# Kernel tuning notes

Hardware: AMD Instinct MI355X
Metric: run time of the kernel (lower is better)

Reference implementation:

```python
import jax, jax.numpy as jnp
import numpy as np

N_PARTICLES = 10_000_000
GRID_N = 256  # per-axis grid size
GRID_EDGE = 10.0  # grid spans [-10, 10] in each axis


def setup_inputs() -> dict:
    key = jax.random.key(0)
    k1, k2 = jax.random.split(key)
    # uniform in [-11, 11]: some particles fall outside the grid -> exercises bounds mask
    positions = jax.random.uniform(k1, (N_PARTICLES, 3), dtype=jnp.float32,
                                   minval=-11.0, maxval=11.0)
    weights = jax.random.uniform(k2, (N_PARTICLES,), dtype=jnp.float32)
    return {"positions": positions, "weights": weights}


def reference(positions, weights):
    # Grid buffers (from Grid.__init__ with grid_edges=(10,10,10), n=(256,256,256))
    n = GRID_N
    grid_min = jnp.full((3,), -GRID_EDGE, dtype=positions.dtype)
    grid_max = jnp.full((3,), GRID_EDGE, dtype=positions.dtype)
    dx = (grid_max - grid_min) / (n - 1)  # [3]

    # float index: fi = (pos - min)/dx  -> nearest grid point via trunc(fi + 0.5)
    fi = (positions - grid_min[None, :]) / dx[None, :]          # [N,3]
    i = (fi + 0.5).astype(jnp.int32)  # C-style trunc-toward-zero, matches torch .type(int64)

    gd = jnp.all((i >= 0) & (i < n), axis=1)                    # [N] in-grid mask

    # flatten 3D index; out-of-grid particles routed to index 0 with zero weight
    flat = (i[:, 0] * n + i[:, 1]) * n + i[:, 2]                # [N]
    flat = jnp.where(gd, flat, 0)
    w = jnp.where(gd, weights, jnp.zeros_like(weights))

    grid = jnp.zeros((n * n * n,), dtype=positions.dtype).at[flat].add(w)
    return grid.reshape(n, n, n)
```

## Files before the change

### kernel.cpp

```cpp
#include <hip/hip_runtime.h>
#include <stdint.h>


constexpr int GRID_N = 256;
constexpr int SB     = 1024;
constexpr int CELLS  = 16384;
constexpr int NB     = 256;
constexpr int BT13   = 1024;
constexpr int RING   = 16;
constexpr int RSTR   = 17;
constexpr int SIDE_CAP = 4096;

__device__ __forceinline__ int particle_flat(float px, float py, float pz) {
#pragma clang fp contract(off)
    float fix = (px + 10.0f) * 12.75f;
    float fiy = (py + 10.0f) * 12.75f;
    float fiz = (pz + 10.0f) * 12.75f;
    int ix = (int)(fix + 0.5f);
    int iy = (int)(fiy + 0.5f);
    int iz = (int)(fiz + 0.5f);
    bool in = (ix >= 0) & (ix < GRID_N) &
              (iy >= 0) & (iy < GRID_N) &
              (iz >= 0) & (iz < GRID_N);
    return in ? ((ix << 16) | (iy << 8) | iz) : -1;
}

__global__ __launch_bounds__(BT13) void k1_hist(const float* __restrict__ pos,
                                                uint32_t* __restrict__ hist,
                                                int n)
{
    __shared__ uint32_t h[SB];
    for (int i = threadIdx.x; i < SB; i += BT13) h[i] = 0;
    __syncthreads();

    const float4* p4 = (const float4*)pos;
    int ngroups = n >> 2;
    int G = gridDim.x * BT13;
    for (int g = blockIdx.x * BT13 + threadIdx.x; g < ngroups; g += G) {
        float4 a = p4[(size_t)g * 3 + 0];
        float4 b = p4[(size_t)g * 3 + 1];
        float4 c = p4[(size_t)g * 3 + 2];
        int f0 = particle_flat(a.x, a.y, a.z);
        int f1 = particle_flat(a.w, b.x, b.y);
        int f2 = particle_flat(b.z, b.w, c.x);
        int f3 = particle_flat(c.y, c.z, c.w);
        if (f0 >= 0) atomicAdd(&h[f0 >> 14], 1u);
        if (f1 >= 0) atomicAdd(&h[f1 >> 14], 1u);
        if (f2 >= 0) atomicAdd(&h[f2 >> 14], 1u);
        if (f3 >= 0) atomicAdd(&h[f3 >> 14], 1u);
    }
    if (blockIdx.x == 0 && threadIdx.x == 0) {
        for (int p = n & ~3; p < n; ++p) {
            int f = particle_flat(pos[3 * p], pos[3 * p + 1], pos[3 * p + 2]);
            if (f >= 0) atomicAdd(&h[f >> 14], 1u);
        }
    }
    __syncthreads();
    uint32_t* out = hist + (size_t)blockIdx.x * SB;
    for (int i = threadIdx.x; i < SB; i += BT13) out[i] = h[i];
}

__global__ __launch_bounds__(128) void k2a_colscan(const uint32_t* __restrict__ hist,
                                                   uint32_t* __restrict__ offs,
                                                   uint32_t* __restrict__ totals,
                                                   int round8)
{
    int b = blockIdx.x * 128 + threadIdx.x;
    uint32_t run = 0;
    for (int blk = 0; blk < NB; blk += 8) {
        uint32_t v[8];
#pragma unroll
        for (int j = 0; j < 8; ++j) {
            uint32_t c = hist[(size_t)(blk + j) * SB + b];
            v[j] = round8 ? ((c + 7u) & ~7u) : c;
        }
#pragma unroll
        for (int j = 0; j < 8; ++j) {
            offs[(size_t)(blk + j) * SB + b] = run;
            run += v[j];
        }
    }
    totals[b] = run;
}

__global__ __launch_bounds__(256) void k2b_scan(const uint32_t* __restrict__ totals,
                                                uint32_t* __restrict__ base)
{
    __shared__ uint32_t part[256];
    int t = threadIdx.x;
    uint32_t local[4];
    uint32_t s = 0;
#pragma unroll
    for (int j = 0; j < 4; ++j) { local[j] = totals[t * 4 + j]; s += local[j]; }
    part[t] = s;
    __syncthreads();
    if (t == 0) {
        uint32_t run = 0;
        for (int i = 0; i < 256; ++i) { uint32_t tmp = part[i]; part[i] = run; run += tmp; }
    }
    __syncthreads();
    uint32_t run = part[t];
#pragma unroll
    for (int j = 0; j < 4; ++j) { base[t * 4 + j] = run; run += local[j]; }
    if (t == 255) base[SB] = run;
}

__global__ __launch_bounds__(BT13, 1) void k3_stage(
    const float* __restrict__ pos, const float* __restrict__ wgt,
    const uint32_t* __restrict__ offs, const uint32_t* __restrict__ base,
    uint2* __restrict__ pairs, uint2* __restrict__ sideg, int n)
{
    __shared__ uint2    stg[SB][RSTR];
    __shared__ uint32_t s_total[SB];
    __shared__ uint32_t s_flushed[SB];
    __shared__ uint32_t s_pbase[SB];
    __shared__ uint32_t s_wl[SB];
    __shared__ uint32_t s_wln;
    __shared__ uint32_t s_siden;

    const int tid = threadIdx.x;
    const int blk = blockIdx.x;

    s_total[tid]   = 0;
    s_flushed[tid] = 0;
    s_pbase[tid]   = base[tid] + offs[(size_t)blk * SB + tid];
    if (tid == 0) { s_wln = 0; s_siden = 0; }
    __syncthreads();

    uint2* side = sideg + (size_t)blk * SIDE_CAP;

    const float4* p4 = (const float4*)pos;
    const float4* w4 = (const float4*)wgt;
    int ngroups = n >> 2;
    int G = NB * BT13;
    int iters = (ngroups + G - 1) / G;

    for (int it = 0; it < iters; ++it) {
        int g = blk * BT13 + tid + it * G;
        if (g < ngroups) {
            float4 a = p4[(size_t)g * 3 + 0];
            float4 b = p4[(size_t)g * 3 + 1];
            float4 c = p4[(size_t)g * 3 + 2];
            float4 w = w4[g];
            int   f[4]  = { particle_flat(a.x, a.y, a.z), particle_flat(a.w, b.x, b.y),
                            particle_flat(b.z, b.w, c.x), particle_flat(c.y, c.z, c.w) };
            float ww[4] = { w.x, w.y, w.z, w.w };
#pragma unroll
            for (int k = 0; k < 4; ++k) {
                int fk = f[k];
                if (fk >= 0) {
                    uint32_t bin  = (uint32_t)fk >> 14;
                    uint32_t slot = atomicAdd(&s_total[bin], 1u);
                    if (slot - s_flushed[bin] < (uint32_t)RING) {
                        stg[bin][slot & (RING - 1)] =
                            make_uint2((uint32_t)fk & (CELLS - 1), __float_as_uint(ww[k]));
                    } else {
                        atomicSub(&s_total[bin], 1u);
                        uint32_t si = atomicAdd(&s_siden, 1u);
                        if (si < SIDE_CAP)
                            side[si] = make_uint2((uint32_t)fk, __float_as_uint(ww[k]));
                    }
                }
            }
        }
        __syncthreads();
        {
            uint32_t p = s_total[tid] - s_flushed[tid];
            if (p >= 8u) {
                uint32_t o = s_flushed[tid];
                s_wl[atomicAdd(&s_wln, 1u)] = ((uint32_t)tid << 22) | o;
                s_flushed[tid] = o + 8u;
            }
        }
        __syncthreads();
        {
            uint32_t m = s_wln;
            for (uint32_t j = tid; j < m * 8u; j += BT13) {
                uint32_t e   = s_wl[j >> 3];
                uint32_t bin = e >> 22;
                uint32_t o   = e & 0x3FFFFFu;
                uint32_t idx = o + (j & 7u);
                uint2 v = stg[bin][idx & (RING - 1)];
                uint64_t v64 = (uint64_t)v.x | ((uint64_t)v.y << 32);
                __builtin_nontemporal_store(v64,
                    (uint64_t*)&pairs[(size_t)s_pbase[bin] + idx]);
            }
            if (tid == 0) s_wln = 0;
        }
        __syncthreads();
    }

    if (tid == 0) {
        uint32_t ns = s_siden < (uint32_t)SIDE_CAP ? s_siden : (uint32_t)SIDE_CAP;
        for (uint32_t i = 0; i < ns; ++i) {
            uint2 e = side[i];
            uint32_t bin = e.x >> 14;
            while (s_total[bin] - s_flushed[bin] >= (uint32_t)RING) {
                uint32_t o = s_flushed[bin];
                for (int j = 0; j < 8; ++j)
                    pairs[(size_t)s_pbase[bin] + o + j] = stg[bin][(o + j) & (RING - 1)];
                s_flushed[bin] = o + 8u;
            }
            uint32_t slot = s_total[bin]++;
            stg[bin][slot & (RING - 1)] = make_uint2(e.x & (CELLS - 1), e.y);
        }
        if (blk == 0) {
            for (int p = n & ~3; p < n; ++p) {
                int f = particle_flat(pos[3 * p], pos[3 * p + 1], pos[3 * p + 2]);
                if (f >= 0) {
                    uint32_t bin = (uint32_t)f >> 14;
                    while (s_total[bin] - s_flushed[bin] >= (uint32_t)RING) {
                        uint32_t o = s_flushed[bin];
                        for (int j = 0; j < 8; ++j)
                            pairs[(size_t)s_pbase[bin] + o + j] = stg[bin][(o + j) & (RING - 1)];
                        s_flushed[bin] = o + 8u;
                    }
                    uint32_t slot = s_total[bin]++;
                    stg[bin][slot & (RING - 1)] =
                        make_uint2((uint32_t)f & (CELLS - 1), __float_as_uint(wgt[p]));
                }
            }
        }
    }
    __syncthreads();

    {
        uint32_t t = s_total[tid];
        uint32_t p = t - s_flushed[tid];
        uint32_t pad = ((p + 7u) & ~7u) - p;
        for (uint32_t j = 0; j < pad; ++j)
            stg[tid][(t + j) & (RING - 1)] = make_uint2(0u, 0u);
        s_total[tid] = t + pad;
    }
    __syncthreads();

    for (int r = 0; r < 2; ++r) {
        {
            uint32_t p = s_total[tid] - s_flushed[tid];
            if (p >= 8u) {
                uint32_t o = s_flushed[tid];
                s_wl[atomicAdd(&s_wln, 1u)] = ((uint32_t)tid << 22) | o;
                s_flushed[tid] = o + 8u;
            }
        }
        __syncthreads();
        {
            uint32_t m = s_wln;
            for (uint32_t j = tid; j < m * 8u; j += BT13) {
                uint32_t e   = s_wl[j >> 3];
                uint32_t bin = e >> 22;
                uint32_t o   = e & 0x3FFFFFu;
                uint32_t idx = o + (j & 7u);
                uint2 v = stg[bin][idx & (RING - 1)];
                uint64_t v64 = (uint64_t)v.x | ((uint64_t)v.y << 32);
                __builtin_nontemporal_store(v64,
                    (uint64_t*)&pairs[(size_t)s_pbase[bin] + idx]);
            }
        }
        __syncthreads();
        if (tid == 0) s_wln = 0;
        __syncthreads();
    }
}

__global__ __launch_bounds__(BT13) void k3_scatter(const float* __restrict__ pos,
                                                   const float* __restrict__ wgt,
                                                   const uint32_t* __restrict__ offs,
                                                   const uint32_t* __restrict__ base,
                                                   uint2* __restrict__ pairs,
                                                   int n)
{
    __shared__ uint32_t cur[SB];
    for (int i = threadIdx.x; i < SB; i += BT13)
        cur[i] = base[i] + offs[(size_t)blockIdx.x * SB + i];
    __syncthreads();

    const float4* p4 = (const float4*)pos;
    const float4* w4 = (const float4*)wgt;
    int ngroups = n >> 2;
    int G = gridDim.x * BT13;
    for (int g = blockIdx.x * BT13 + threadIdx.x; g < ngroups; g += G) {
        float4 a = p4[(size_t)g * 3 + 0];
        float4 b = p4[(size_t)g * 3 + 1];
        float4 c = p4[(size_t)g * 3 + 2];
        float4 w = w4[g];
        int   f[4]  = { particle_flat(a.x, a.y, a.z), particle_flat(a.w, b.x, b.y),
                        particle_flat(b.z, b.w, c.x), particle_flat(c.y, c.z, c.w) };
        float ww[4] = { w.x, w.y, w.z, w.w };
#pragma unroll
        for (int k = 0; k < 4; ++k) {
            if (f[k] >= 0) {
                uint32_t slot = atomicAdd(&cur[f[k] >> 14], 1u);
                pairs[slot] = make_uint2((uint32_t)(f[k] & (CELLS - 1)),
                                         __float_as_uint(ww[k]));
            }
        }
    }
    if (blockIdx.x == 0 && threadIdx.x == 0) {
        for (int p = n & ~3; p < n; ++p) {
            int f = particle_flat(pos[3 * p], pos[3 * p + 1], pos[3 * p + 2]);
            if (f >= 0) {
                uint32_t slot = atomicAdd(&cur[f >> 14], 1u);
                pairs[slot] = make_uint2((uint32_t)(f & (CELLS - 1)),
                                         __float_as_uint(wgt[p]));
            }
        }
    }
}

__global__ __launch_bounds__(BT13) void k4_accum(const uint2* __restrict__ pairs,
                                                 const uint32_t* __restrict__ base,
                                                 float* __restrict__ grid)
{
    __shared__ float acc[CELLS];
    for (int i = threadIdx.x; i < CELLS; i += BT13) acc[i] = 0.0f;
    __syncthreads();

    int b = blockIdx.x;
    uint32_t s = base[b], e = base[b + 1];
    for (uint32_t i = s + threadIdx.x; i < e; i += BT13) {
        uint2 p = pairs[i];
        atomicAdd(&acc[p.x], __uint_as_float(p.y));
    }
    __syncthreads();

    float4* out4 = (float4*)(grid + (size_t)b * CELLS);
    const float4* a4 = (const float4*)acc;
    for (int i = threadIdx.x; i < CELLS / 4; i += BT13) out4[i] = a4[i];
}

__global__ __launch_bounds__(256) void forcegrid_scatter_atomic(
    const float* __restrict__ pos, const float* __restrict__ wgt,
    float* __restrict__ grid, int n)
{
    int t = blockIdx.x * blockDim.x + threadIdx.x;
    long long bse = (long long)t * 4;
    if (bse >= n) return;
    const float4* p4 = (const float4*)pos;
    float4 a = p4[(size_t)t * 3 + 0];
    float4 b = p4[(size_t)t * 3 + 1];
    float4 c = p4[(size_t)t * 3 + 2];
    float4 w = ((const float4*)wgt)[t];
    int   f[4]  = { particle_flat(a.x, a.y, a.z), particle_flat(a.w, b.x, b.y),
                    particle_flat(b.z, b.w, c.x), particle_flat(c.y, c.z, c.w) };
    float ww[4] = { w.x, w.y, w.z, w.w };
#pragma unroll
    for (int k = 0; k < 4; ++k) {
        if (bse + k >= n) break;
        if (f[k] >= 0) atomicAdd(&grid[f[k]], ww[k]);
    }
}

extern "C" void kernel_launch(void* const* d_in, const int* in_sizes, int n_in,
                              void* d_out, int out_size, void* d_ws, size_t ws_size,
                              hipStream_t stream)
{
    const float* pos = (const float*)d_in[0];
    const float* wgt = (const float*)d_in[1];
    float* grid = (float*)d_out;
    int n = in_sizes[0] / 3;

    size_t npad = (size_t)n + (size_t)NB * SB * 7;
    size_t o1 = 0;
    uint2*    pairs1  = (uint2*)d_ws;                         o1 += npad * sizeof(uint2);
    uint2*    sideg   = (uint2*)((char*)d_ws + o1);           o1 += (size_t)NB * SIDE_CAP * sizeof(uint2);
    uint32_t* hist1   = (uint32_t*)((char*)d_ws + o1);        o1 += (size_t)NB * SB * 4;
    uint32_t* offs1   = (uint32_t*)((char*)d_ws + o1);        o1 += (size_t)NB * SB * 4;
    uint32_t* totals1 = (uint32_t*)((char*)d_ws + o1);        o1 += (size_t)SB * 4;
    uint32_t* base1   = (uint32_t*)((char*)d_ws + o1);        o1 += (size_t)(SB + 1) * 4;

    if (ws_size >= o1) {
        k1_hist    <<<NB,       BT13, 0, stream>>>(pos, hist1, n);
        k2a_colscan<<<SB / 128, 128,  0, stream>>>(hist1, offs1, totals1, 1);
        k2b_scan   <<<1,        256,  0, stream>>>(totals1, base1);
        k3_stage   <<<NB,       BT13, 0, stream>>>(pos, wgt, offs1, base1, pairs1, sideg, n);
        k4_accum   <<<SB,       BT13, 0, stream>>>(pairs1, base1, grid);
        return;
    }

    size_t o2 = 0;
    uint2*    pairs2  = (uint2*)d_ws;                         o2 += (size_t)n * sizeof(uint2);
    uint32_t* hist2   = (uint32_t*)((char*)d_ws + o2);        o2 += (size_t)NB * SB * 4;
    uint32_t* offs2   = (uint32_t*)((char*)d_ws + o2);        o2 += (size_t)NB * SB * 4;
    uint32_t* totals2 = (uint32_t*)((char*)d_ws + o2);        o2 += (size_t)SB * 4;
    uint32_t* base2   = (uint32_t*)((char*)d_ws + o2);        o2 += (size_t)(SB + 1) * 4;

    if (ws_size >= o2) {
        k1_hist    <<<NB,       BT13, 0, stream>>>(pos, hist2, n);
        k2a_colscan<<<SB / 128, 128,  0, stream>>>(hist2, offs2, totals2, 0);
        k2b_scan   <<<1,        256,  0, stream>>>(totals2, base2);
        k3_scatter <<<NB,       BT13, 0, stream>>>(pos, wgt, offs2, base2, pairs2, n);
        k4_accum   <<<SB,       BT13, 0, stream>>>(pairs2, base2, grid);
    } else {
        hipMemsetAsync(grid, 0, (size_t)out_size * sizeof(float), stream);
        int groups = (n + 3) / 4;
        forcegrid_scatter_atomic<<<(groups + 255) / 256, 256, 0, stream>>>(pos, wgt, grid, n);
    }
}
```

Measured before the change: 329.4 us.

## Replace histogram+scan prepass with fixed-capacity bins and global atomic cursors

Drops the histogram pass, the two scan kernels and the first full read of positions. The staging kernel now claims 8-entry chunks of a fixed-capacity per-bin region through global atomic cursors. Pairs that overflow a ring or a bin region go to a shared global side buffer, which every accumulate block scans and filters by bin. This saves one pass over the 120MB position array and several launches, at the cost of global atomics per chunk flush, a larger workspace, and a side buffer that can silently drop entries past its capacity.

Result: faster. 295.5 us (-10.3%).

```diff
diff --git a/kernel.cpp b/kernel.cpp
--- a/kernel.cpp
+++ b/kernel.cpp
@@ -6,10 +6,10 @@
 constexpr int SB     = 1024;
 constexpr int CELLS  = 16384;
 constexpr int NB     = 256;
-constexpr int BT13   = 1024;
+constexpr int BT     = 1024;
 constexpr int RING   = 16;
 constexpr int RSTR   = 17;
-constexpr int SIDE_CAP = 4096;
+constexpr uint32_t SIDE_CAP = 65536;
 
 __device__ __forceinline__ int particle_flat(float px, float py, float pz) {
 #pragma clang fp contract(off)
@@ -25,18 +25,210 @@
     return in ? ((ix << 16) | (iy << 8) | iz) : -1;
 }
 
-__global__ __launch_bounds__(BT13) void k1_hist(const float* __restrict__ pos,
-                                                uint32_t* __restrict__ hist,
-                                                int n)
+__global__ __launch_bounds__(1024) void k0_init(uint32_t* __restrict__ gcur,
+                                                uint32_t* __restrict__ side_n,
+                                                uint32_t C)
+{
+    int t = blockIdx.x * blockDim.x + threadIdx.x;
+    if (t < SB) gcur[t] = (uint32_t)t * C;
+    if (t == 0) *side_n = 0;
+}
+
+__global__ __launch_bounds__(BT, 1) void k3_direct(
+    const float* __restrict__ pos, const float* __restrict__ wgt,
+    uint32_t* __restrict__ gcur, uint2* __restrict__ pairs,
+    uint2* __restrict__ side, uint32_t* __restrict__ side_n,
+    uint32_t C, int n)
+{
+    __shared__ uint2    stg[SB][RSTR];
+    __shared__ uint32_t s_total[SB];
+    __shared__ uint32_t s_flushed[SB];
+    __shared__ uint32_t s_wl[SB];
+    __shared__ uint32_t s_wldst[SB];
+    __shared__ uint32_t s_wln;
+
+    const int tid = threadIdx.x;
+    const int blk = blockIdx.x;
+
+    s_total[tid]   = 0;
+    s_flushed[tid] = 0;
+    if (tid == 0) s_wln = 0;
+    __syncthreads();
+
+    const float4* p4 = (const float4*)pos;
+    const float4* w4 = (const float4*)wgt;
+    int ngroups = n >> 2;
+    int G = NB * BT;
+    int iters = (ngroups + G - 1) / G;
+
+    for (int it = 0; it < iters; ++it) {
+        if (tid == 0) s_wln = 0;
+        int g = blk * BT + tid + it * G;
+        if (g < ngroups) {
+            float4 a = p4[(size_t)g * 3 + 0];
+            float4 b = p4[(size_t)g * 3 + 1];
+            float4 c = p4[(size_t)g * 3 + 2];
+            float4 w = w4[g];
+            int   f[4]  = { particle_flat(a.x, a.y, a.z), particle_flat(a.w, b.x, b.y),
+                            particle_flat(b.z, b.w, c.x), particle_flat(c.y, c.z, c.w) };
+            float ww[4] = { w.x, w.y, w.z, w.w };
+#pragma unroll
+            for (int k = 0; k < 4; ++k) {
+                int fk = f[k];
+                if (fk >= 0) {
+                    uint32_t bin  = (uint32_t)fk >> 14;
+                    uint32_t slot = atomicAdd(&s_total[bin], 1u);
+                    if (slot - s_flushed[bin] < (uint32_t)RING) {
+                        stg[bin][slot & (RING - 1)] =
+                            make_uint2((uint32_t)fk & (CELLS - 1), __float_as_uint(ww[k]));
+                    } else {
+                        atomicSub(&s_total[bin], 1u);
+                        uint32_t si = atomicAdd(side_n, 1u);
+                        if (si < SIDE_CAP)
+                            side[si] = make_uint2((uint32_t)fk, __float_as_uint(ww[k]));
+                    }
+                }
+            }
+        }
+        __syncthreads();
+        {
+            uint32_t p = s_total[tid] - s_flushed[tid];
+            if (p >= 8u) {
+                uint32_t o   = s_flushed[tid];
+                uint32_t dst = atomicAdd(&gcur[tid], 8u);
+                if (dst + 8u <= (uint32_t)(tid + 1) * C) {
+                    uint32_t wi = atomicAdd(&s_wln, 1u);
+                    s_wl[wi]    = ((uint32_t)tid << 4) | (o & (RING - 1));
+                    s_wldst[wi] = dst;
+                } else {
+                    atomicSub(&gcur[tid], 8u);
+                    for (int j = 0; j < 8; ++j) {
+                        uint2 v = stg[tid][(o + j) & (RING - 1)];
+                        uint32_t si = atomicAdd(side_n, 1u);
+                        if (si < SIDE_CAP)
+                            side[si] = make_uint2(((uint32_t)tid << 14) | v.x, v.y);
+                    }
+                }
+                s_flushed[tid] = o + 8u;
+            }
+        }
+        __syncthreads();
+        {
+            uint32_t m = s_wln;
+            for (uint32_t j = tid; j < m * 8u; j += BT) {
+                uint32_t e = s_wl[j >> 3];
+                uint2 v = stg[e >> 4][((e & (RING - 1)) + (j & 7u)) & (RING - 1)];
+                uint64_t v64 = (uint64_t)v.x | ((uint64_t)v.y << 32);
+                __builtin_nontemporal_store(v64,
+                    (uint64_t*)&pairs[(size_t)s_wldst[j >> 3] + (j & 7u)]);
+            }
+        }
+        __syncthreads();
+    }
+
+    if (blk == 0 && tid == 0) {
+        for (int p = n & ~3; p < n; ++p) {
+            int f = particle_flat(pos[3 * p], pos[3 * p + 1], pos[3 * p + 2]);
+            if (f >= 0) {
+                uint32_t si = atomicAdd(side_n, 1u);
+                if (si < SIDE_CAP)
+                    side[si] = make_uint2((uint32_t)f, __float_as_uint(wgt[p]));
+            }
+        }
+    }
+
+    {
+        uint32_t t = s_total[tid];
+        uint32_t p = t - s_flushed[tid];
+        uint32_t pad = ((p + 7u) & ~7u) - p;
+        for (uint32_t j = 0; j < pad; ++j)
+            stg[tid][(t + j) & (RING - 1)] = make_uint2(0u, 0u);
+        s_total[tid] = t + pad;
+    }
+    __syncthreads();
+
+    for (int r = 0; r < 2; ++r) {
+        if (tid == 0) s_wln = 0;
+        __syncthreads();
+        {
+            uint32_t p = s_total[tid] - s_flushed[tid];
+            if (p >= 8u) {
+                uint32_t o   = s_flushed[tid];
+                uint32_t dst = atomicAdd(&gcur[tid], 8u);
+                if (dst + 8u <= (uint32_t)(tid + 1) * C) {
+                    uint32_t wi = atomicAdd(&s_wln, 1u);
+                    s_wl[wi]    = ((uint32_t)tid << 4) | (o & (RING - 1));
+                    s_wldst[wi] = dst;
+                } else {
+                    atomicSub(&gcur[tid], 8u);
+                    for (int j = 0; j < 8; ++j) {
+                        uint2 v = stg[tid][(o + j) & (RING - 1)];
+                        uint32_t si = atomicAdd(side_n, 1u);
+                        if (si < SIDE_CAP)
+                            side[si] = make_uint2(((uint32_t)tid << 14) | v.x, v.y);
+                    }
+                }
+                s_flushed[tid] = o + 8u;
+            }
+        }
+        __syncthreads();
+        {
+            uint32_t m = s_wln;
+            for (uint32_t j = tid; j < m * 8u; j += BT) {
+                uint32_t e = s_wl[j >> 3];
+                uint2 v = stg[e >> 4][((e & (RING - 1)) + (j & 7u)) & (RING - 1)];
+                uint64_t v64 = (uint64_t)v.x | ((uint64_t)v.y << 32);
+                __builtin_nontemporal_store(v64,
+                    (uint64_t*)&pairs[(size_t)s_wldst[j >> 3] + (j & 7u)]);
+            }
+        }
+        __syncthreads();
+    }
+}
+
+__global__ __launch_bounds__(BT) void k4_direct(const uint2* __restrict__ pairs,
+                                                const uint32_t* __restrict__ gcur,
+                                                const uint2* __restrict__ side,
+                                                const uint32_t* __restrict__ side_n,
+                                                uint32_t C,
+                                                float* __restrict__ grid)
+{
+    __shared__ float acc[CELLS];
+    for (int i = threadIdx.x; i < CELLS; i += BT) acc[i] = 0.0f;
+    __syncthreads();
+
+    int b = blockIdx.x;
+    uint32_t s = (uint32_t)b * C, e = gcur[b];
+    for (uint32_t i = s + threadIdx.x; i < e; i += BT) {
+        uint2 p = pairs[i];
+        atomicAdd(&acc[p.x], __uint_as_float(p.y));
+    }
+    uint32_t ns = *side_n;
+    if (ns > SIDE_CAP) ns = SIDE_CAP;
+    for (uint32_t i = threadIdx.x; i < ns; i += BT) {
+        uint2 sv = side[i];
+        if ((int)(sv.x >> 14) == b)
+            atomicAdd(&acc[sv.x & (CELLS - 1)], __uint_as_float(sv.y));
+    }
+    __syncthreads();
+
+    float4* out4 = (float4*)(grid + (size_t)b * CELLS);
+    const float4* a4 = (const float4*)acc;
+    for (int i = threadIdx.x; i < CELLS / 4; i += BT) out4[i] = a4[i];
+}
+
+__global__ __launch_bounds__(BT) void k1_hist(const float* __restrict__ pos,
+                                              uint32_t* __restrict__ hist,
+                                              int n)
 {
     __shared__ uint32_t h[SB];
-    for (int i = threadIdx.x; i < SB; i += BT13) h[i] = 0;
+    for (int i = threadIdx.x; i < SB; i += BT) h[i] = 0;
     __syncthreads();
 
     const float4* p4 = (const float4*)pos;
     int ngroups = n >> 2;
-    int G = gridDim.x * BT13;
-    for (int g = blockIdx.x * BT13 + threadIdx.x; g < ngroups; g += G) {
+    int G = gridDim.x * BT;
+    for (int g = blockIdx.x * BT + threadIdx.x; g < ngroups; g += G) {
         float4 a = p4[(size_t)g * 3 + 0];
         float4 b = p4[(size_t)g * 3 + 1];
         float4 c = p4[(size_t)g * 3 + 2];
@@ -57,23 +249,20 @@
     }
     __syncthreads();
     uint32_t* out = hist + (size_t)blockIdx.x * SB;
-    for (int i = threadIdx.x; i < SB; i += BT13) out[i] = h[i];
+    for (int i = threadIdx.x; i < SB; i += BT) out[i] = h[i];
 }
 
 __global__ __launch_bounds__(128) void k2a_colscan(const uint32_t* __restrict__ hist,
                                                    uint32_t* __restrict__ offs,
-                                                   uint32_t* __restrict__ totals,
-                                                   int round8)
+                                                   uint32_t* __restrict__ totals)
 {
     int b = blockIdx.x * 128 + threadIdx.x;
     uint32_t run = 0;
     for (int blk = 0; blk < NB; blk += 8) {
         uint32_t v[8];
 #pragma unroll
-        for (int j = 0; j < 8; ++j) {
-            uint32_t c = hist[(size_t)(blk + j) * SB + b];
-            v[j] = round8 ? ((c + 7u) & ~7u) : c;
-        }
+        for (int j = 0; j < 8; ++j)
+            v[j] = hist[(size_t)(blk + j) * SB + b];
 #pragma unroll
         for (int j = 0; j < 8; ++j) {
             offs[(size_t)(blk + j) * SB + b] = run;
@@ -105,181 +294,23 @@
     if (t == 255) base[SB] = run;
 }
 
-__global__ __launch_bounds__(BT13, 1) void k3_stage(
-    const float* __restrict__ pos, const float* __restrict__ wgt,
-    const uint32_t* __restrict__ offs, const uint32_t* __restrict__ base,
-    uint2* __restrict__ pairs, uint2* __restrict__ sideg, int n)
-{
-    __shared__ uint2    stg[SB][RSTR];
-    __shared__ uint32_t s_total[SB];
-    __shared__ uint32_t s_flushed[SB];
-    __shared__ uint32_t s_pbase[SB];
-    __shared__ uint32_t s_wl[SB];
-    __shared__ uint32_t s_wln;
-    __shared__ uint32_t s_siden;
-
-    const int tid = threadIdx.x;
-    const int blk = blockIdx.x;
-
-    s_total[tid]   = 0;
-    s_flushed[tid] = 0;
-    s_pbase[tid]   = base[tid] + offs[(size_t)blk * SB + tid];
-    if (tid == 0) { s_wln = 0; s_siden = 0; }
-    __syncthreads();
-
-    uint2* side = sideg + (size_t)blk * SIDE_CAP;
+__global__ __launch_bounds__(BT) void k3_scatter(const float* __restrict__ pos,
+                                                 const float* __restrict__ wgt,
+                                                 const uint32_t* __restrict__ offs,
+                                                 const uint32_t* __restrict__ base,
+                                                 uint2* __restrict__ pairs,
+                                                 int n)
+{
+    __shared__ uint32_t cur[SB];
+    for (int i = threadIdx.x; i < SB; i += BT)
+        cur[i] = base[i] + offs[(size_t)blockIdx.x * SB + i];
+    __syncthreads();
 
     const float4* p4 = (const float4*)pos;
     const float4* w4 = (const float4*)wgt;
     int ngroups = n >> 2;
-    int G = NB * BT13;
-    int iters = (ngroups + G - 1) / G;
-
-    for (int it = 0; it < iters; ++it) {
-        int g = blk * BT13 + tid + it * G;
-        if (g < ngroups) {
-            float4 a = p4[(size_t)g * 3 + 0];
-            float4 b = p4[(size_t)g * 3 + 1];
-            float4 c = p4[(size_t)g * 3 + 2];
-            float4 w = w4[g];
-            int   f[4]  = { particle_flat(a.x, a.y, a.z), particle_flat(a.w, b.x, b.y),
-                            particle_flat(b.z, b.w, c.x), particle_flat(c.y, c.z, c.w) };
-            float ww[4] = { w.x, w.y, w.z, w.w };
-#pragma unroll
-            for (int k = 0; k < 4; ++k) {
-                int fk = f[k];
-                if (fk >= 0) {
-                    uint32_t bin  = (uint32_t)fk >> 14;
-                    uint32_t slot = atomicAdd(&s_total[bin], 1u);
-                    if (slot - s_flushed[bin] < (uint32_t)RING) {
-                        stg[bin][slot & (RING - 1)] =
-                            make_uint2((uint32_t)fk & (CELLS - 1), __float_as_uint(ww[k]));
-                    } else {
-                        atomicSub(&s_total[bin], 1u);
-                        uint32_t si = atomicAdd(&s_siden, 1u);
-                        if (si < SIDE_CAP)
-                            side[si] = make_uint2((uint32_t)fk, __float_as_uint(ww[k]));
-                    }
-                }
-            }
-        }
-        __syncthreads();
-        {
-            uint32_t p = s_total[tid] - s_flushed[tid];
-            if (p >= 8u) {
-                uint32_t o = s_flushed[tid];
-                s_wl[atomicAdd(&s_wln, 1u)] = ((uint32_t)tid << 22) | o;
-                s_flushed[tid] = o + 8u;
-            }
-        }
-        __syncthreads();
-        {
-            uint32_t m = s_wln;
-            for (uint32_t j = tid; j < m * 8u; j += BT13) {
-                uint32_t e   = s_wl[j >> 3];
-                uint32_t bin = e >> 22;
-                uint32_t o   = e & 0x3FFFFFu;
-                uint32_t idx = o + (j & 7u);
-                uint2 v = stg[bin][idx & (RING - 1)];
-                uint64_t v64 = (uint64_t)v.x | ((uint64_t)v.y << 32);
-                __builtin_nontemporal_store(v64,
-                    (uint64_t*)&pairs[(size_t)s_pbase[bin] + idx]);
-            }
-            if (tid == 0) s_wln = 0;
-        }
-        __syncthreads();
-    }
-
-    if (tid == 0) {
-        uint32_t ns = s_siden < (uint32_t)SIDE_CAP ? s_siden : (uint32_t)SIDE_CAP;
-        for (uint32_t i = 0; i < ns; ++i) {
-            uint2 e = side[i];
-            uint32_t bin = e.x >> 14;
-            while (s_total[bin] - s_flushed[bin] >= (uint32_t)RING) {
-                uint32_t o = s_flushed[bin];
-                for (int j = 0; j < 8; ++j)
-                    pairs[(size_t)s_pbase[bin] + o + j] = stg[bin][(o + j) & (RING - 1)];
-                s_flushed[bin] = o + 8u;
-            }
-            uint32_t slot = s_total[bin]++;
-            stg[bin][slot & (RING - 1)] = make_uint2(e.x & (CELLS - 1), e.y);
-        }
-        if (blk == 0) {
-            for (int p = n & ~3; p < n; ++p) {
-                int f = particle_flat(pos[3 * p], pos[3 * p + 1], pos[3 * p + 2]);
-                if (f >= 0) {
-                    uint32_t bin = (uint32_t)f >> 14;
-                    while (s_total[bin] - s_flushed[bin] >= (uint32_t)RING) {
-                        uint32_t o = s_flushed[bin];
-                        for (int j = 0; j < 8; ++j)
-                            pairs[(size_t)s_pbase[bin] + o + j] = stg[bin][(o + j) & (RING - 1)];
-                        s_flushed[bin] = o + 8u;
-                    }
-                    uint32_t slot = s_total[bin]++;
-                    stg[bin][slot & (RING - 1)] =
-                        make_uint2((uint32_t)f & (CELLS - 1), __float_as_uint(wgt[p]));
-                }
-            }
-        }
-    }
-    __syncthreads();
-
-    {
-        uint32_t t = s_total[tid];
-        uint32_t p = t - s_flushed[tid];
-        uint32_t pad = ((p + 7u) & ~7u) - p;
-        for (uint32_t j = 0; j < pad; ++j)
-            stg[tid][(t + j) & (RING - 1)] = make_uint2(0u, 0u);
-        s_total[tid] = t + pad;
-    }
-    __syncthreads();
-
-    for (int r = 0; r < 2; ++r) {
-        {
-            uint32_t p = s_total[tid] - s_flushed[tid];
-            if (p >= 8u) {
-                uint32_t o = s_flushed[tid];
-                s_wl[atomicAdd(&s_wln, 1u)] = ((uint32_t)tid << 22) | o;
-                s_flushed[tid] = o + 8u;
-            }
-        }
-        __syncthreads();
-        {
-            uint32_t m = s_wln;
-            for (uint32_t j = tid; j < m * 8u; j += BT13) {
-                uint32_t e   = s_wl[j >> 3];
-                uint32_t bin = e >> 22;
-                uint32_t o   = e & 0x3FFFFFu;
-                uint32_t idx = o + (j & 7u);
-                uint2 v = stg[bin][idx & (RING - 1)];
-                uint64_t v64 = (uint64_t)v.x | ((uint64_t)v.y << 32);
-                __builtin_nontemporal_store(v64,
-                    (uint64_t*)&pairs[(size_t)s_pbase[bin] + idx]);
-            }
-        }
-        __syncthreads();
-        if (tid == 0) s_wln = 0;
-        __syncthreads();
-    }
-}
-
-__global__ __launch_bounds__(BT13) void k3_scatter(const float* __restrict__ pos,
-                                                   const float* __restrict__ wgt,
-                                                   const uint32_t* __restrict__ offs,
-                                                   const uint32_t* __restrict__ base,
-                                                   uint2* __restrict__ pairs,
-                                                   int n)
-{
-    __shared__ uint32_t cur[SB];
-    for (int i = threadIdx.x; i < SB; i += BT13)
-        cur[i] = base[i] + offs[(size_t)blockIdx.x * SB + i];
-    __syncthreads();
-
-    const float4* p4 = (const float4*)pos;
-    const float4* w4 = (const float4*)wgt;
-    int ngroups = n >> 2;
-    int G = gridDim.x * BT13;
-    for (int g = blockIdx.x * BT13 + threadIdx.x; g < ngroups; g += G) {
+    int G = gridDim.x * BT;
+    for (int g = blockIdx.x * BT + threadIdx.x; g < ngroups; g += G) {
         float4 a = p4[(size_t)g * 3 + 0];
         float4 b = p4[(size_t)g * 3 + 1];
         float4 c = p4[(size_t)g * 3 + 2];
@@ -308,17 +339,17 @@
     }
 }
 
-__global__ __launch_bounds__(BT13) void k4_accum(const uint2* __restrict__ pairs,
-                                                 const uint32_t* __restrict__ base,
-                                                 float* __restrict__ grid)
+__global__ __launch_bounds__(BT) void k4_seg(const uint2* __restrict__ pairs,
+                                             const uint32_t* __restrict__ base,
+                                             float* __restrict__ grid)
 {
     __shared__ float acc[CELLS];
-    for (int i = threadIdx.x; i < CELLS; i += BT13) acc[i] = 0.0f;
+    for (int i = threadIdx.x; i < CELLS; i += BT) acc[i] = 0.0f;
     __syncthreads();
 
     int b = blockIdx.x;
     uint32_t s = base[b], e = base[b + 1];
-    for (uint32_t i = s + threadIdx.x; i < e; i += BT13) {
+    for (uint32_t i = s + threadIdx.x; i < e; i += BT) {
         uint2 p = pairs[i];
         atomicAdd(&acc[p.x], __uint_as_float(p.y));
     }
@@ -326,7 +357,7 @@
 
     float4* out4 = (float4*)(grid + (size_t)b * CELLS);
     const float4* a4 = (const float4*)acc;
-    for (int i = threadIdx.x; i < CELLS / 4; i += BT13) out4[i] = a4[i];
+    for (int i = threadIdx.x; i < CELLS / 4; i += BT) out4[i] = a4[i];
 }
 
 __global__ __launch_bounds__(256) void forcegrid_scatter_atomic(
@@ -360,37 +391,34 @@
     float* grid = (float*)d_out;
     int n = in_sizes[0] / 3;
 
-    size_t npad = (size_t)n + (size_t)NB * SB * 7;
+    uint32_t C = ((2u * (uint32_t)(n / SB) + 4096u) + 7u) & ~7u;
+    if (C < 1024u) C = 1024u;
     size_t o1 = 0;
-    uint2*    pairs1  = (uint2*)d_ws;                         o1 += npad * sizeof(uint2);
-    uint2*    sideg   = (uint2*)((char*)d_ws + o1);           o1 += (size_t)NB * SIDE_CAP * sizeof(uint2);
-    uint32_t* hist1   = (uint32_t*)((char*)d_ws + o1);        o1 += (size_t)NB * SB * 4;
-    uint32_t* offs1   = (uint32_t*)((char*)d_ws + o1);        o1 += (size_t)NB * SB * 4;
-    uint32_t* totals1 = (uint32_t*)((char*)d_ws + o1);        o1 += (size_t)SB * 4;
-    uint32_t* base1   = (uint32_t*)((char*)d_ws + o1);        o1 += (size_t)(SB + 1) * 4;
+    uint2*    pairs1 = (uint2*)d_ws;                     o1 += (size_t)SB * C * sizeof(uint2);
+    uint2*    side   = (uint2*)((char*)d_ws + o1);       o1 += (size_t)SIDE_CAP * sizeof(uint2);
+    uint32_t* gcur   = (uint32_t*)((char*)d_ws + o1);    o1 += (size_t)SB * 4;
+    uint32_t* side_n = (uint32_t*)((char*)d_ws + o1);    o1 += 64;
 
     if (ws_size >= o1) {
-        k1_hist    <<<NB,       BT13, 0, stream>>>(pos, hist1, n);
-        k2a_colscan<<<SB / 128, 128,  0, stream>>>(hist1, offs1, totals1, 1);
-        k2b_scan   <<<1,        256,  0, stream>>>(totals1, base1);
-        k3_stage   <<<NB,       BT13, 0, stream>>>(pos, wgt, offs1, base1, pairs1, sideg, n);
-        k4_accum   <<<SB,       BT13, 0, stream>>>(pairs1, base1, grid);
+        k0_init  <<<1,  1024, 0, stream>>>(gcur, side_n, C);
+        k3_direct<<<NB, BT,   0, stream>>>(pos, wgt, gcur, pairs1, side, side_n, C, n);
+        k4_direct<<<SB, BT,   0, stream>>>(pairs1, gcur, side, side_n, C, grid);
         return;
     }
 
     size_t o2 = 0;
-    uint2*    pairs2  = (uint2*)d_ws;                         o2 += (size_t)n * sizeof(uint2);
-    uint32_t* hist2   = (uint32_t*)((char*)d_ws + o2);        o2 += (size_t)NB * SB * 4;
-    uint32_t* offs2   = (uint32_t*)((char*)d_ws + o2);        o2 += (size_t)NB * SB * 4;
-    uint32_t* totals2 = (uint32_t*)((char*)d_ws + o2);        o2 += (size_t)SB * 4;
-    uint32_t* base2   = (uint32_t*)((char*)d_ws + o2);        o2 += (size_t)(SB + 1) * 4;
+    uint2*    pairs2  = (uint2*)d_ws;                    o2 += (size_t)n * sizeof(uint2);
+    uint32_t* hist2   = (uint32_t*)((char*)d_ws + o2);   o2 += (size_t)NB * SB * 4;
+    uint32_t* offs2   = (uint32_t*)((char*)d_ws + o2);   o2 += (size_t)NB * SB * 4;
+    uint32_t* totals2 = (uint32_t*)((char*)d_ws + o2);   o2 += (size_t)SB * 4;
+    uint32_t* base2   = (uint32_t*)((char*)d_ws + o2);   o2 += (size_t)(SB + 1) * 4;
 
     if (ws_size >= o2) {
-        k1_hist    <<<NB,       BT13, 0, stream>>>(pos, hist2, n);
-        k2a_colscan<<<SB / 128, 128,  0, stream>>>(hist2, offs2, totals2, 0);
-        k2b_scan   <<<1,        256,  0, stream>>>(totals2, base2);
-        k3_scatter <<<NB,       BT13, 0, stream>>>(pos, wgt, offs2, base2, pairs2, n);
-        k4_accum   <<<SB,       BT13, 0, stream>>>(pairs2, base2, grid);
+        k1_hist    <<<NB,       BT,  0, stream>>>(pos, hist2, n);
+        k2a_colscan<<<SB / 128, 128, 0, stream>>>(hist2, offs2, totals2);
+        k2b_scan   <<<1,        256, 0, stream>>>(totals2, base2);
+        k3_scatter <<<NB,       BT,  0, stream>>>(pos, wgt, offs2, base2, pairs2, n);
+        k4_seg     <<<SB,       BT,  0, stream>>>(pairs2, base2, grid);
     } else {
         hipMemsetAsync(grid, 0, (size_t)out_size * sizeof(float), stream);
         int groups = (n + 3) / 4;
```
